# Kernel tuning notes

Measured on AMD Instinct MI355X. Metric: run time of the kernel, lower is better.

Reference implementation:

```python
import jax, jax.numpy as jnp
import numpy as np

N = 50000      # nodes
E = 800000     # edges
IN = 128       # in_channels
H = 128        # hidden_channels
OUT = 500      # out_channels
EPS = 1e-5


def setup_inputs() -> dict:
    key = jax.random.key(0)
    ks = jax.random.split(key, 8)
    def rn(k, shape, scale=0.05):
        return jax.random.normal(k, shape, jnp.float32) * scale
    return {
        "x": jax.random.normal(ks[0], (N, IN), jnp.float32),
        "edge_index": jax.random.randint(ks[1], (2, E), 0, N, dtype=jnp.int32),
        "W1": rn(ks[2], (IN, H)), "b1": jnp.zeros((H,), jnp.float32),
        "g1": jnp.ones((H,), jnp.float32), "be1": jnp.zeros((H,), jnp.float32),
        "W2": rn(ks[3], (H, 2 * H)), "b2": jnp.zeros((2 * H,), jnp.float32),
        "g2": jnp.ones((2 * H,), jnp.float32), "be2": jnp.zeros((2 * H,), jnp.float32),
        "W3": rn(ks[4], (2 * H, H)), "b3": jnp.zeros((H,), jnp.float32),
        "g3": jnp.ones((H,), jnp.float32), "be3": jnp.zeros((H,), jnp.float32),
        "Wl1": rn(ks[5], (H, H // 2)), "bl1": jnp.zeros((H // 2,), jnp.float32),
        "g4": jnp.ones((H // 2,), jnp.float32), "be4": jnp.zeros((H // 2,), jnp.float32),
        "Wl2": rn(ks[6], (H // 2, OUT)), "bl2": jnp.zeros((OUT,), jnp.float32),
    }


def layer_norm(x, g, b):
    mu = jnp.mean(x, axis=-1, keepdims=True)
    var = jnp.mean(jnp.square(x - mu), axis=-1, keepdims=True)
    return (x - mu) * jax.lax.rsqrt(var + EPS) * g + b


def gcn_conv(x, W, b, src, dst, n):
    # PyG GCNConv: x' = D^{-1/2} (A + I) D^{-1/2} (x W) + b, with self-loops.
    h = x @ W                                   # [N, F]
    ones = jnp.ones(src.shape[0], h.dtype)
    deg = jax.ops.segment_sum(ones, dst, num_segments=n) + 1.0  # +1 self-loop
    dinv = jnp.where(deg > 0, jax.lax.rsqrt(deg), 0.0)          # [N]
    coef = dinv[src] * dinv[dst]                # [E]
    agg = jax.ops.segment_sum(h[src] * coef[:, None], dst, num_segments=n)
    agg = agg + h * jnp.square(dinv)[:, None]   # self-loop messages
    return agg + b


def reference(x, edge_index, W1, b1, g1, be1, W2, b2, g2, be2,
              W3, b3, g3, be3, Wl1, bl1, g4, be4, Wl2, bl2):
    # eval mode: dropout is identity
    src, dst = edge_index[0], edge_index[1]
    n = x.shape[0]
    h = jax.nn.elu(layer_norm(gcn_conv(x, W1, b1, src, dst, n), g1, be1))
    h = jax.nn.elu(layer_norm(gcn_conv(h, W2, b2, src, dst, n), g2, be2))
    h = jax.nn.elu(layer_norm(gcn_conv(h, W3, b3, src, dst, n), g3, be3))
    h = jax.nn.elu(layer_norm(h @ Wl1 + bl1, g4, be4))
    return h @ Wl2 + bl2
```

## Files before the change

kernel.cpp:

```cpp
#include <hip/hip_runtime.h>
#include <cstdint>


#define LN_EPS 1e-5f

typedef __attribute__((ext_vector_type(8))) short bf16x8;
typedef __attribute__((ext_vector_type(4))) float f32x4;

static __device__ __forceinline__ ushort f2bf(float f) {
  union { float f; uint u; } c; c.f = f;
  uint u = c.u;
  return (ushort)((u + 0x7fffu + ((u >> 16) & 1u)) >> 16);
}
static __device__ __forceinline__ float bf2f(ushort h) {
  union { uint u; float f; } c; c.u = (uint)h << 16;
  return c.f;
}


__global__ void zero1_kernel(int* __restrict__ a, int n) {
  int i = blockIdx.x * blockDim.x + threadIdx.x;
  if (i < n) a[i] = 0;
}

__global__ void deg_kernel(const int* __restrict__ dst, int* __restrict__ deg, int E) {
  int e = blockIdx.x * blockDim.x + threadIdx.x;
  if (e < E) atomicAdd(&deg[dst[e]], 1);
}

__global__ void scan1_kernel(const int* __restrict__ deg, int* __restrict__ excl,
                             int* __restrict__ bsums, float* __restrict__ dinv, int N) {
  __shared__ int s[256];
  int tid = threadIdx.x;
  int i = blockIdx.x * 256 + tid;
  int v = (i < N) ? deg[i] : 0;
  s[tid] = v;
  __syncthreads();
  for (int o = 1; o < 256; o <<= 1) {
    int t = (tid >= o) ? s[tid - o] : 0;
    __syncthreads();
    if (tid >= o) s[tid] += t;
    __syncthreads();
  }
  if (i < N) {
    excl[i] = s[tid] - v;
    dinv[i] = rsqrtf((float)v + 1.0f);
  }
  if (tid == 255) bsums[blockIdx.x] = s[tid];
}

__global__ void scan2_kernel(int* __restrict__ bsums, int nb) {
  __shared__ int s[256];
  int tid = threadIdx.x;
  int v = (tid < nb) ? bsums[tid] : 0;
  s[tid] = v;
  __syncthreads();
  for (int o = 1; o < 256; o <<= 1) {
    int t = (tid >= o) ? s[tid - o] : 0;
    __syncthreads();
    if (tid >= o) s[tid] += t;
    __syncthreads();
  }
  if (tid < nb) bsums[tid] = s[tid] - v;
}

__global__ void scan3_kernel(int* __restrict__ rowptr, int* __restrict__ fill,
                             const int* __restrict__ bsums, int N, int Etotal) {
  int i = blockIdx.x * blockDim.x + threadIdx.x;
  if (i < N) {
    int v = rowptr[i] + bsums[i >> 8];
    rowptr[i] = v;
    fill[i] = v;
  } else if (i == N) {
    rowptr[N] = Etotal;
  }
}

__global__ void fill_kernel(const int* __restrict__ src, const int* __restrict__ dst,
                            int* __restrict__ fill, int* __restrict__ srcs, int E) {
  int e = blockIdx.x * blockDim.x + threadIdx.x;
  if (e >= E) return;
  int idx = atomicAdd(&fill[dst[e]], 1);
  srcs[idx] = src[e];
}


__global__ void f2bf_vec_kernel(const float* __restrict__ in, ushort* __restrict__ out, int n4) {
  int i = blockIdx.x * blockDim.x + threadIdx.x;
  if (i >= n4) return;
  float4 v = ((const float4*)in)[i];
  ushort4 o;
  o.x = f2bf(v.x); o.y = f2bf(v.y); o.z = f2bf(v.z); o.w = f2bf(v.w);
  ((ushort4*)out)[i] = o;
}

struct WConvArgs {
  const float* w[5];
  ushort* wt[5];
  int K[5], N[5];
  int off[6];
};

__global__ void wconv_kernel(WConvArgs a, int total) {
  int i = blockIdx.x * blockDim.x + threadIdx.x;
  if (i >= total) return;
  int m = 0;
  while (i >= a.off[m + 1]) m++;
  int j = i - a.off[m];
  int k = j / a.N[m], n = j - k * a.N[m];
  a.wt[m][(size_t)n * a.K[m] + k] = f2bf(a.w[m][j]);
}

#define TBM 128
#define TBN 128
#define TBK 32
#define LDK 40

template <bool OUT_BF16>
__global__ __launch_bounds__(256, 2) void mfma_gemm_kernel(
    const ushort* __restrict__ A, const ushort* __restrict__ Bt,
    const float* __restrict__ bias, void* __restrict__ Cout,
    int M, int N, int K) {
  __shared__ ushort As[TBM][LDK];
  __shared__ ushort Bs[TBN][LDK];
  const int tid = threadIdx.x;
  const int lane = tid & 63;
  const int w = tid >> 6;
  const int wm = w & 1, wn = w >> 1;
  const int quad = lane >> 4, l16 = lane & 15;
  const int rowBase = blockIdx.y * TBM;
  const int colBase = blockIdx.x * TBN;

  f32x4 acc[4][4] = {};
  const int lr = tid >> 2;
  const int lk = (tid & 3) * 8;

  for (int k0 = 0; k0 < K; k0 += TBK) {
#pragma unroll
    for (int h = 0; h < 2; h++) {
      int r = lr + h * 64;
      int grow = rowBase + r;
      uint4 va = make_uint4(0, 0, 0, 0);
      if (grow < M) va = *(const uint4*)(A + (size_t)grow * K + k0 + lk);
      *(uint4*)&As[r][lk] = va;
      int gcol = colBase + r;
      uint4 vb = make_uint4(0, 0, 0, 0);
      if (gcol < N) vb = *(const uint4*)(Bt + (size_t)gcol * K + k0 + lk);
      *(uint4*)&Bs[r][lk] = vb;
    }
    __syncthreads();
    bf16x8 af[4], bfr[4];
#pragma unroll
    for (int i = 0; i < 4; i++) {
      af[i]  = *(const bf16x8*)&As[wm * 64 + i * 16 + l16][quad * 8];
      bfr[i] = *(const bf16x8*)&Bs[wn * 64 + i * 16 + l16][quad * 8];
    }
#pragma unroll
    for (int i = 0; i < 4; i++)
#pragma unroll
      for (int j = 0; j < 4; j++)
        acc[i][j] = __builtin_amdgcn_mfma_f32_16x16x32_bf16(af[i], bfr[j], acc[i][j], 0, 0, 0);
    __syncthreads();
  }
#pragma unroll
  for (int i = 0; i < 4; i++) {
    int row0 = rowBase + wm * 64 + i * 16 + quad * 4;
#pragma unroll
    for (int j = 0; j < 4; j++) {
      int col = colBase + wn * 64 + j * 16 + l16;
      if (col >= N) continue;
      float bv = bias ? bias[col] : 0.f;
#pragma unroll
      for (int r = 0; r < 4; r++) {
        int row = row0 + r;
        if (row >= M) continue;
        float v = acc[i][j][r] + bv;
        if (OUT_BF16) ((ushort*)Cout)[(size_t)row * N + col] = f2bf(v);
        else          ((float*)Cout)[(size_t)row * N + col] = v;
      }
    }
  }
}


__global__ __launch_bounds__(256) void agg_kernel(
    const ushort* __restrict__ hb, const int* __restrict__ rowptr,
    const int* __restrict__ srcs, const float* __restrict__ dinv,
    uint* __restrict__ out, int Nn) {
  const int wave = threadIdx.x >> 6;
  const int n = blockIdx.x * 4 + wave;
  if (n >= Nn) return;
  const int f = threadIdx.x & 63;
  const uint* h32 = (const uint*)hb;
  const float di = dinv[n];
  uint self = h32[(size_t)n * 64 + f];
  float a0 = bf2f((ushort)(self & 0xffffu)) * di * di;
  float a1 = bf2f((ushort)(self >> 16)) * di * di;
  int i = rowptr[n];
  const int e = rowptr[n + 1];
  for (; i + 3 < e; i += 4) {
    int s0 = srcs[i], s1 = srcs[i + 1], s2 = srcs[i + 2], s3 = srcs[i + 3];
    float c0 = dinv[s0] * di, c1 = dinv[s1] * di, c2 = dinv[s2] * di, c3 = dinv[s3] * di;
    uint v0 = h32[(size_t)s0 * 64 + f];
    uint v1 = h32[(size_t)s1 * 64 + f];
    uint v2 = h32[(size_t)s2 * 64 + f];
    uint v3 = h32[(size_t)s3 * 64 + f];
    a0 += c0 * bf2f((ushort)(v0 & 0xffffu)) + c1 * bf2f((ushort)(v1 & 0xffffu)) +
          c2 * bf2f((ushort)(v2 & 0xffffu)) + c3 * bf2f((ushort)(v3 & 0xffffu));
    a1 += c0 * bf2f((ushort)(v0 >> 16)) + c1 * bf2f((ushort)(v1 >> 16)) +
          c2 * bf2f((ushort)(v2 >> 16)) + c3 * bf2f((ushort)(v3 >> 16));
  }
  for (; i < e; i++) {
    int s = srcs[i];
    float c = dinv[s] * di;
    uint v = h32[(size_t)s * 64 + f];
    a0 += c * bf2f((ushort)(v & 0xffffu));
    a1 += c * bf2f((ushort)(v >> 16));
  }
  out[(size_t)n * 64 + f] = (uint)f2bf(a0) | ((uint)f2bf(a1) << 16);
}

__global__ __launch_bounds__(256) void agg_ln_kernel(
    const ushort* __restrict__ hb, const int* __restrict__ rowptr,
    const int* __restrict__ srcs, const float* __restrict__ dinv,
    const float* __restrict__ bias, const float* __restrict__ g,
    const float* __restrict__ be, uint* __restrict__ out, int Nn) {
  const int wave = threadIdx.x >> 6;
  const int n = blockIdx.x * 4 + wave;
  if (n >= Nn) return;
  const int f = threadIdx.x & 63;
  const uint* h32 = (const uint*)hb;
  const float di = dinv[n];
  uint self = h32[(size_t)n * 64 + f];
  float2 bv = ((const float2*)bias)[f];
  float a0 = bf2f((ushort)(self & 0xffffu)) * di * di + bv.x;
  float a1 = bf2f((ushort)(self >> 16)) * di * di + bv.y;
  int i = rowptr[n];
  const int e = rowptr[n + 1];
  for (; i + 3 < e; i += 4) {
    int s0 = srcs[i], s1 = srcs[i + 1], s2 = srcs[i + 2], s3 = srcs[i + 3];
    float c0 = dinv[s0] * di, c1 = dinv[s1] * di, c2 = dinv[s2] * di, c3 = dinv[s3] * di;
    uint v0 = h32[(size_t)s0 * 64 + f];
    uint v1 = h32[(size_t)s1 * 64 + f];
    uint v2 = h32[(size_t)s2 * 64 + f];
    uint v3 = h32[(size_t)s3 * 64 + f];
    a0 += c0 * bf2f((ushort)(v0 & 0xffffu)) + c1 * bf2f((ushort)(v1 & 0xffffu)) +
          c2 * bf2f((ushort)(v2 & 0xffffu)) + c3 * bf2f((ushort)(v3 & 0xffffu));
    a1 += c0 * bf2f((ushort)(v0 >> 16)) + c1 * bf2f((ushort)(v1 >> 16)) +
          c2 * bf2f((ushort)(v2 >> 16)) + c3 * bf2f((ushort)(v3 >> 16));
  }
  for (; i < e; i++) {
    int s = srcs[i];
    float c = dinv[s] * di;
    uint v = h32[(size_t)s * 64 + f];
    a0 += c * bf2f((ushort)(v & 0xffffu));
    a1 += c * bf2f((ushort)(v >> 16));
  }
  float s = a0 + a1;
#pragma unroll
  for (int o = 32; o >= 1; o >>= 1) s += __shfl_xor(s, o);
  float mean = s * (1.0f / 128.0f);
  float d0 = a0 - mean, d1 = a1 - mean;
  float q = d0 * d0 + d1 * d1;
#pragma unroll
  for (int o = 32; o >= 1; o >>= 1) q += __shfl_xor(q, o);
  float rstd = rsqrtf(q * (1.0f / 128.0f) + LN_EPS);
  float2 gv = ((const float2*)g)[f];
  float2 bev = ((const float2*)be)[f];
  float y0 = d0 * rstd * gv.x + bev.x;
  float y1 = d1 * rstd * gv.y + bev.y;
  y0 = (y0 > 0.f) ? y0 : expm1f(y0);
  y1 = (y1 > 0.f) ? y1 : expm1f(y1);
  out[(size_t)n * 64 + f] = (uint)f2bf(y0) | ((uint)f2bf(y1) << 16);
}

template <int F, bool IN_BF16>
__global__ __launch_bounds__(F) void ln_elu_kernel(const void* __restrict__ xin,
                                                   const float* __restrict__ g,
                                                   const float* __restrict__ be,
                                                   ushort* __restrict__ out) {
  constexpr int NW = (F + 63) / 64;
  __shared__ float sb[NW];
  const int row = blockIdx.x;
  const int f = threadIdx.x;
  float v;
  if (IN_BF16) v = bf2f(((const ushort*)xin)[(size_t)row * F + f]);
  else         v = ((const float*)xin)[(size_t)row * F + f];
  float s = v;
#pragma unroll
  for (int o = 32; o >= 1; o >>= 1) s += __shfl_xor(s, o);
  float mean;
  if constexpr (NW == 1) {
    mean = s * (1.0f / F);
  } else {
    if ((f & 63) == 0) sb[f >> 6] = s;
    __syncthreads();
    float t = 0.f;
#pragma unroll
    for (int w2 = 0; w2 < NW; w2++) t += sb[w2];
    mean = t * (1.0f / F);
    __syncthreads();
  }
  float d = v - mean;
  float q = d * d;
#pragma unroll
  for (int o = 32; o >= 1; o >>= 1) q += __shfl_xor(q, o);
  float var;
  if constexpr (NW == 1) {
    var = q * (1.0f / F);
  } else {
    if ((f & 63) == 0) sb[f >> 6] = q;
    __syncthreads();
    float t = 0.f;
#pragma unroll
    for (int w2 = 0; w2 < NW; w2++) t += sb[w2];
    var = t * (1.0f / F);
  }
  float y = d * rsqrtf(var + LN_EPS) * g[f] + be[f];
  out[(size_t)row * F + f] = f2bf((y > 0.f) ? y : expm1f(y));
}


extern "C" void kernel_launch(void* const* d_in, const int* in_sizes, int n_in,
                              void* d_out, int out_size, void* d_ws, size_t ws_size,
                              hipStream_t stream) {
  const float* x   = (const float*)d_in[0];
  const int*   ei  = (const int*)d_in[1];
  const float* W1  = (const float*)d_in[2];
  const float* b1  = (const float*)d_in[3];
  const float* g1  = (const float*)d_in[4];
  const float* be1 = (const float*)d_in[5];
  const float* W2  = (const float*)d_in[6];
  const float* b2  = (const float*)d_in[7];
  const float* g2  = (const float*)d_in[8];
  const float* be2 = (const float*)d_in[9];
  const float* W3  = (const float*)d_in[10];
  const float* b3  = (const float*)d_in[11];
  const float* g3  = (const float*)d_in[12];
  const float* be3 = (const float*)d_in[13];
  const float* Wl1 = (const float*)d_in[14];
  const float* bl1 = (const float*)d_in[15];
  const float* g4  = (const float*)d_in[16];
  const float* be4 = (const float*)d_in[17];
  const float* Wl2 = (const float*)d_in[18];
  const float* bl2 = (const float*)d_in[19];

  const int N = in_sizes[0] / 128;
  const int E = in_sizes[1] / 2;
  const int* esrc = ei;
  const int* edst = ei + E;

  char* p = (char*)d_ws;
  float* F1 = (float*)p;              p += (size_t)N * 128 * 4;
  ushort* Pb = (ushort*)p;            p += (size_t)N * 256 * 2;
  ushort* Qb = (ushort*)p;            p += (size_t)N * 256 * 2;
  ushort* W1t = (ushort*)p;           p += 128 * 128 * 2;
  ushort* W2t = (ushort*)p;           p += 128 * 256 * 2;
  ushort* W3t = (ushort*)p;           p += 256 * 128 * 2;
  ushort* Wl1t = (ushort*)p;          p += 128 * 64 * 2;
  ushort* Wl2t = (ushort*)p;          p += 64 * 500 * 2;
  int*   srcs  = (int*)p;             p += (size_t)E * 4;
  int*   deg   = (int*)p;             p += (size_t)N * 4;
  float* dinv  = (float*)p;           p += (size_t)N * 4;
  int*   rowptr= (int*)p;             p += (size_t)(N + 2) * 4;
  int*   fill  = (int*)p;             p += (size_t)N * 4;
  int*   bsums = (int*)p;             p += 256 * 4;
  ushort* xb = (ushort*)F1;

  const int nb = (N + 255) / 256;
  const int eb = (E + 255) / 256;

  zero1_kernel<<<nb, 256, 0, stream>>>(deg, N);
  deg_kernel<<<eb, 256, 0, stream>>>(edst, deg, E);
  scan1_kernel<<<nb, 256, 0, stream>>>(deg, rowptr, bsums, dinv, N);
  scan2_kernel<<<1, 256, 0, stream>>>(bsums, nb);
  scan3_kernel<<<(N + 256) / 256, 256, 0, stream>>>(rowptr, fill, bsums, N, E);
  fill_kernel<<<eb, 256, 0, stream>>>(esrc, edst, fill, srcs, E);

  f2bf_vec_kernel<<<(N * 128 / 4 + 255) / 256, 256, 0, stream>>>(x, xb, N * 128 / 4);
  WConvArgs wa;
  wa.w[0] = W1;  wa.wt[0] = W1t;  wa.K[0] = 128; wa.N[0] = 128;
  wa.w[1] = W2;  wa.wt[1] = W2t;  wa.K[1] = 128; wa.N[1] = 256;
  wa.w[2] = W3;  wa.wt[2] = W3t;  wa.K[2] = 256; wa.N[2] = 128;
  wa.w[3] = Wl1; wa.wt[3] = Wl1t; wa.K[3] = 128; wa.N[3] = 64;
  wa.w[4] = Wl2; wa.wt[4] = Wl2t; wa.K[4] = 64;  wa.N[4] = 500;
  wa.off[0] = 0;
  for (int m = 0; m < 5; m++) wa.off[m + 1] = wa.off[m] + wa.K[m] * wa.N[m];
  int wtotal = wa.off[5];
  wconv_kernel<<<(wtotal + 255) / 256, 256, 0, stream>>>(wa, wtotal);

  auto gemm_bf = [&](const ushort* A, const ushort* Bt, const float* bias, ushort* C,
                     int M, int Nn, int K) {
    dim3 grid((Nn + TBN - 1) / TBN, (M + TBM - 1) / TBM);
    mfma_gemm_kernel<true><<<grid, 256, 0, stream>>>(A, Bt, bias, C, M, Nn, K);
  };
  auto gemm_f32 = [&](const ushort* A, const ushort* Bt, const float* bias, float* C,
                      int M, int Nn, int K) {
    dim3 grid((Nn + TBN - 1) / TBN, (M + TBM - 1) / TBM);
    mfma_gemm_kernel<false><<<grid, 256, 0, stream>>>(A, Bt, bias, C, M, Nn, K);
  };
  const int ab = (N + 3) / 4;

  gemm_bf(xb, W1t, nullptr, Pb, N, 128, 128);
  agg_ln_kernel<<<ab, 256, 0, stream>>>(Pb, rowptr, srcs, dinv, b1, g1, be1, (uint*)Qb, N);

  agg_kernel<<<ab, 256, 0, stream>>>(Qb, rowptr, srcs, dinv, (uint*)Pb, N);
  gemm_bf(Pb, W2t, b2, Qb, N, 256, 128);
  ln_elu_kernel<256, true><<<N, 256, 0, stream>>>(Qb, g2, be2, Pb);

  gemm_bf(Pb, W3t, nullptr, Qb, N, 128, 256);
  agg_ln_kernel<<<ab, 256, 0, stream>>>(Qb, rowptr, srcs, dinv, b3, g3, be3, (uint*)Pb, N);

  gemm_f32(Pb, Wl1t, bl1, F1, N, 64, 128);
  ln_elu_kernel<64, false><<<N, 64, 0, stream>>>(F1, g4, be4, Qb);

  gemm_f32(Qb, Wl2t, bl2, (float*)d_out, N, 500, 64);
}
```

Before: 529.7 us.

## Fuse fp32-to-bf16 input cast into GEMM, vectorize aggregation gathers, repack LN kernels

The first GEMM now reads fp32 x directly and converts to bf16 while staging into shared memory, which removes the separate conversion kernel and its round trip through memory. The aggregation kernels become one template that gives 4 edges per wave, with 16 lanes per edge loading 16-byte uint4 rows, and reduces across lanes with shuffles. This cuts the number of gather instructions but leaves three quarters of the lanes idle at the final store. The 64-wide LayerNorm kernel now packs four rows per block instead of using 64-thread blocks.

```diff
diff --git a/kernel.cpp b/kernel.cpp
--- a/kernel.cpp
+++ b/kernel.cpp
@@ -14,6 +14,14 @@
 }
 static __device__ __forceinline__ float bf2f(ushort h) {
   union { uint u; float f; } c; c.u = (uint)h << 16;
+  return c.f;
+}
+static __device__ __forceinline__ float bflo(uint u) {
+  union { uint u; float f; } c; c.u = u << 16;
+  return c.f;
+}
+static __device__ __forceinline__ float bfhi(uint u) {
+  union { uint u; float f; } c; c.u = u & 0xffff0000u;
   return c.f;
 }
 
@@ -85,15 +93,6 @@
 }
 
 
-__global__ void f2bf_vec_kernel(const float* __restrict__ in, ushort* __restrict__ out, int n4) {
-  int i = blockIdx.x * blockDim.x + threadIdx.x;
-  if (i >= n4) return;
-  float4 v = ((const float4*)in)[i];
-  ushort4 o;
-  o.x = f2bf(v.x); o.y = f2bf(v.y); o.z = f2bf(v.z); o.w = f2bf(v.w);
-  ((ushort4*)out)[i] = o;
-}
-
 struct WConvArgs {
   const float* w[5];
   ushort* wt[5];
@@ -116,9 +115,9 @@
 #define TBK 32
 #define LDK 40
 
-template <bool OUT_BF16>
+template <bool A_FP32, bool OUT_BF16>
 __global__ __launch_bounds__(256, 2) void mfma_gemm_kernel(
-    const ushort* __restrict__ A, const ushort* __restrict__ Bt,
+    const void* __restrict__ Ain, const ushort* __restrict__ Bt,
     const float* __restrict__ bias, void* __restrict__ Cout,
     int M, int N, int K) {
   __shared__ ushort As[TBM][LDK];
@@ -132,21 +131,45 @@
   const int colBase = blockIdx.x * TBN;
 
   f32x4 acc[4][4] = {};
-  const int lr = tid >> 2;
-  const int lk = (tid & 3) * 8;
+  const int sr = tid >> 1;
+  const int sk = (tid & 1) * 16;
 
   for (int k0 = 0; k0 < K; k0 += TBK) {
-#pragma unroll
-    for (int h = 0; h < 2; h++) {
-      int r = lr + h * 64;
-      int grow = rowBase + r;
-      uint4 va = make_uint4(0, 0, 0, 0);
-      if (grow < M) va = *(const uint4*)(A + (size_t)grow * K + k0 + lk);
-      *(uint4*)&As[r][lk] = va;
-      int gcol = colBase + r;
-      uint4 vb = make_uint4(0, 0, 0, 0);
-      if (gcol < N) vb = *(const uint4*)(Bt + (size_t)gcol * K + k0 + lk);
-      *(uint4*)&Bs[r][lk] = vb;
+    {
+      int grow = rowBase + sr;
+      if (A_FP32) {
+        const float* Af = (const float*)Ain;
+        float4 f0 = {}, f1 = {}, f2 = {}, f3 = {};
+        if (grow < M) {
+          const float4* ap = (const float4*)(Af + (size_t)grow * K + k0 + sk);
+          f0 = ap[0]; f1 = ap[1]; f2 = ap[2]; f3 = ap[3];
+        }
+        ushort t[16] = {f2bf(f0.x), f2bf(f0.y), f2bf(f0.z), f2bf(f0.w),
+                        f2bf(f1.x), f2bf(f1.y), f2bf(f1.z), f2bf(f1.w),
+                        f2bf(f2.x), f2bf(f2.y), f2bf(f2.z), f2bf(f2.w),
+                        f2bf(f3.x), f2bf(f3.y), f2bf(f3.z), f2bf(f3.w)};
+        *(uint4*)&As[sr][sk] = *(const uint4*)&t[0];
+        *(uint4*)&As[sr][sk + 8] = *(const uint4*)&t[8];
+      } else {
+        const ushort* Ab = (const ushort*)Ain;
+        uint4 v0 = {}, v1 = {};
+        if (grow < M) {
+          const uint4* ap = (const uint4*)(Ab + (size_t)grow * K + k0 + sk);
+          v0 = ap[0]; v1 = ap[1];
+        }
+        *(uint4*)&As[sr][sk] = v0;
+        *(uint4*)&As[sr][sk + 8] = v1;
+      }
+    }
+    {
+      int gcol = colBase + sr;
+      uint4 v0 = {}, v1 = {};
+      if (gcol < N) {
+        const uint4* bp = (const uint4*)(Bt + (size_t)gcol * K + k0 + sk);
+        v0 = bp[0]; v1 = bp[1];
+      }
+      *(uint4*)&Bs[sr][sk] = v0;
+      *(uint4*)&Bs[sr][sk + 8] = v1;
     }
     __syncthreads();
     bf16x8 af[4], bfr[4];
@@ -182,45 +205,8 @@
   }
 }
 
-
+template <bool DO_LN>
 __global__ __launch_bounds__(256) void agg_kernel(
-    const ushort* __restrict__ hb, const int* __restrict__ rowptr,
-    const int* __restrict__ srcs, const float* __restrict__ dinv,
-    uint* __restrict__ out, int Nn) {
-  const int wave = threadIdx.x >> 6;
-  const int n = blockIdx.x * 4 + wave;
-  if (n >= Nn) return;
-  const int f = threadIdx.x & 63;
-  const uint* h32 = (const uint*)hb;
-  const float di = dinv[n];
-  uint self = h32[(size_t)n * 64 + f];
-  float a0 = bf2f((ushort)(self & 0xffffu)) * di * di;
-  float a1 = bf2f((ushort)(self >> 16)) * di * di;
-  int i = rowptr[n];
-  const int e = rowptr[n + 1];
-  for (; i + 3 < e; i += 4) {
-    int s0 = srcs[i], s1 = srcs[i + 1], s2 = srcs[i + 2], s3 = srcs[i + 3];
-    float c0 = dinv[s0] * di, c1 = dinv[s1] * di, c2 = dinv[s2] * di, c3 = dinv[s3] * di;
-    uint v0 = h32[(size_t)s0 * 64 + f];
-    uint v1 = h32[(size_t)s1 * 64 + f];
-    uint v2 = h32[(size_t)s2 * 64 + f];
-    uint v3 = h32[(size_t)s3 * 64 + f];
-    a0 += c0 * bf2f((ushort)(v0 & 0xffffu)) + c1 * bf2f((ushort)(v1 & 0xffffu)) +
-          c2 * bf2f((ushort)(v2 & 0xffffu)) + c3 * bf2f((ushort)(v3 & 0xffffu));
-    a1 += c0 * bf2f((ushort)(v0 >> 16)) + c1 * bf2f((ushort)(v1 >> 16)) +
-          c2 * bf2f((ushort)(v2 >> 16)) + c3 * bf2f((ushort)(v3 >> 16));
-  }
-  for (; i < e; i++) {
-    int s = srcs[i];
-    float c = dinv[s] * di;
-    uint v = h32[(size_t)s * 64 + f];
-    a0 += c * bf2f((ushort)(v & 0xffffu));
-    a1 += c * bf2f((ushort)(v >> 16));
-  }
-  out[(size_t)n * 64 + f] = (uint)f2bf(a0) | ((uint)f2bf(a1) << 16);
-}
-
-__global__ __launch_bounds__(256) void agg_ln_kernel(
     const ushort* __restrict__ hb, const int* __restrict__ rowptr,
     const int* __restrict__ srcs, const float* __restrict__ dinv,
     const float* __restrict__ bias, const float* __restrict__ g,
@@ -228,96 +214,128 @@
   const int wave = threadIdx.x >> 6;
   const int n = blockIdx.x * 4 + wave;
   if (n >= Nn) return;
-  const int f = threadIdx.x & 63;
-  const uint* h32 = (const uint*)hb;
+  const int lane = threadIdx.x & 63;
+  const int slot = lane >> 4;
+  const int sl = lane & 15;
   const float di = dinv[n];
-  uint self = h32[(size_t)n * 64 + f];
-  float2 bv = ((const float2*)bias)[f];
-  float a0 = bf2f((ushort)(self & 0xffffu)) * di * di + bv.x;
-  float a1 = bf2f((ushort)(self >> 16)) * di * di + bv.y;
-  int i = rowptr[n];
-  const int e = rowptr[n + 1];
-  for (; i + 3 < e; i += 4) {
-    int s0 = srcs[i], s1 = srcs[i + 1], s2 = srcs[i + 2], s3 = srcs[i + 3];
-    float c0 = dinv[s0] * di, c1 = dinv[s1] * di, c2 = dinv[s2] * di, c3 = dinv[s3] * di;
-    uint v0 = h32[(size_t)s0 * 64 + f];
-    uint v1 = h32[(size_t)s1 * 64 + f];
-    uint v2 = h32[(size_t)s2 * 64 + f];
-    uint v3 = h32[(size_t)s3 * 64 + f];
-    a0 += c0 * bf2f((ushort)(v0 & 0xffffu)) + c1 * bf2f((ushort)(v1 & 0xffffu)) +
-          c2 * bf2f((ushort)(v2 & 0xffffu)) + c3 * bf2f((ushort)(v3 & 0xffffu));
-    a1 += c0 * bf2f((ushort)(v0 >> 16)) + c1 * bf2f((ushort)(v1 >> 16)) +
-          c2 * bf2f((ushort)(v2 >> 16)) + c3 * bf2f((ushort)(v3 >> 16));
-  }
-  for (; i < e; i++) {
-    int s = srcs[i];
-    float c = dinv[s] * di;
-    uint v = h32[(size_t)s * 64 + f];
-    a0 += c * bf2f((ushort)(v & 0xffffu));
-    a1 += c * bf2f((ushort)(v >> 16));
-  }
-  float s = a0 + a1;
-#pragma unroll
-  for (int o = 32; o >= 1; o >>= 1) s += __shfl_xor(s, o);
-  float mean = s * (1.0f / 128.0f);
-  float d0 = a0 - mean, d1 = a1 - mean;
-  float q = d0 * d0 + d1 * d1;
-#pragma unroll
-  for (int o = 32; o >= 1; o >>= 1) q += __shfl_xor(q, o);
-  float rstd = rsqrtf(q * (1.0f / 128.0f) + LN_EPS);
-  float2 gv = ((const float2*)g)[f];
-  float2 bev = ((const float2*)be)[f];
-  float y0 = d0 * rstd * gv.x + bev.x;
-  float y1 = d1 * rstd * gv.y + bev.y;
-  y0 = (y0 > 0.f) ? y0 : expm1f(y0);
-  y1 = (y1 > 0.f) ? y1 : expm1f(y1);
-  out[(size_t)n * 64 + f] = (uint)f2bf(y0) | ((uint)f2bf(y1) << 16);
-}
-
-template <int F, bool IN_BF16>
-__global__ __launch_bounds__(F) void ln_elu_kernel(const void* __restrict__ xin,
-                                                   const float* __restrict__ g,
-                                                   const float* __restrict__ be,
-                                                   ushort* __restrict__ out) {
-  constexpr int NW = (F + 63) / 64;
-  __shared__ float sb[NW];
+
+  float acc[8] = {};
+  {
+    uint4 v = ((const uint4*)(hb + (size_t)n * 128))[sl];
+    float c = (slot == 0) ? di * di : 0.f;
+    acc[0] = c * bflo(v.x); acc[1] = c * bfhi(v.x);
+    acc[2] = c * bflo(v.y); acc[3] = c * bfhi(v.y);
+    acc[4] = c * bflo(v.z); acc[5] = c * bfhi(v.z);
+    acc[6] = c * bflo(v.w); acc[7] = c * bfhi(v.w);
+  }
+  const int e0 = rowptr[n], e1 = rowptr[n + 1];
+  for (int i = e0; i < e1; i += 8) {
+    int i0 = i + slot, i1 = i + 4 + slot;
+    int s0 = (i0 < e1) ? srcs[i0] : 0;
+    int s1 = (i1 < e1) ? srcs[i1] : 0;
+    float c0 = (i0 < e1) ? dinv[s0] * di : 0.f;
+    float c1 = (i1 < e1) ? dinv[s1] * di : 0.f;
+    uint4 v0 = ((const uint4*)(hb + (size_t)s0 * 128))[sl];
+    uint4 v1 = ((const uint4*)(hb + (size_t)s1 * 128))[sl];
+    acc[0] += c0 * bflo(v0.x) + c1 * bflo(v1.x);
+    acc[1] += c0 * bfhi(v0.x) + c1 * bfhi(v1.x);
+    acc[2] += c0 * bflo(v0.y) + c1 * bflo(v1.y);
+    acc[3] += c0 * bfhi(v0.y) + c1 * bfhi(v1.y);
+    acc[4] += c0 * bflo(v0.z) + c1 * bflo(v1.z);
+    acc[5] += c0 * bfhi(v0.z) + c1 * bfhi(v1.z);
+    acc[6] += c0 * bflo(v0.w) + c1 * bflo(v1.w);
+    acc[7] += c0 * bfhi(v0.w) + c1 * bfhi(v1.w);
+  }
+#pragma unroll
+  for (int j = 0; j < 8; j++) {
+    acc[j] += __shfl_xor(acc[j], 16);
+    acc[j] += __shfl_xor(acc[j], 32);
+  }
+  if (DO_LN) {
+    float4 bv0 = ((const float4*)bias)[2 * sl];
+    float4 bv1 = ((const float4*)bias)[2 * sl + 1];
+    acc[0] += bv0.x; acc[1] += bv0.y; acc[2] += bv0.z; acc[3] += bv0.w;
+    acc[4] += bv1.x; acc[5] += bv1.y; acc[6] += bv1.z; acc[7] += bv1.w;
+    float s = acc[0] + acc[1] + acc[2] + acc[3] + acc[4] + acc[5] + acc[6] + acc[7];
+#pragma unroll
+    for (int o = 1; o <= 8; o <<= 1) s += __shfl_xor(s, o);
+    float mean = s * (1.0f / 128.0f);
+    float q = 0.f;
+#pragma unroll
+    for (int j = 0; j < 8; j++) {
+      acc[j] -= mean;
+      q += acc[j] * acc[j];
+    }
+#pragma unroll
+    for (int o = 1; o <= 8; o <<= 1) q += __shfl_xor(q, o);
+    float rstd = rsqrtf(q * (1.0f / 128.0f) + LN_EPS);
+    float4 gv0 = ((const float4*)g)[2 * sl];
+    float4 gv1 = ((const float4*)g)[2 * sl + 1];
+    float4 ev0 = ((const float4*)be)[2 * sl];
+    float4 ev1 = ((const float4*)be)[2 * sl + 1];
+    float gg[8] = {gv0.x, gv0.y, gv0.z, gv0.w, gv1.x, gv1.y, gv1.z, gv1.w};
+    float ee[8] = {ev0.x, ev0.y, ev0.z, ev0.w, ev1.x, ev1.y, ev1.z, ev1.w};
+#pragma unroll
+    for (int j = 0; j < 8; j++) {
+      float y = acc[j] * rstd * gg[j] + ee[j];
+      acc[j] = (y > 0.f) ? y : expm1f(y);
+    }
+  }
+  if (slot == 0) {
+    uint4 o;
+    o.x = (uint)f2bf(acc[0]) | ((uint)f2bf(acc[1]) << 16);
+    o.y = (uint)f2bf(acc[2]) | ((uint)f2bf(acc[3]) << 16);
+    o.z = (uint)f2bf(acc[4]) | ((uint)f2bf(acc[5]) << 16);
+    o.w = (uint)f2bf(acc[6]) | ((uint)f2bf(acc[7]) << 16);
+    ((uint4*)(out + (size_t)n * 64))[sl] = o;
+  }
+}
+
+
+__global__ __launch_bounds__(256) void ln_elu256_kernel(const ushort* __restrict__ xin,
+                                                        const float* __restrict__ g,
+                                                        const float* __restrict__ be,
+                                                        ushort* __restrict__ out) {
+  __shared__ float sb[4];
   const int row = blockIdx.x;
   const int f = threadIdx.x;
-  float v;
-  if (IN_BF16) v = bf2f(((const ushort*)xin)[(size_t)row * F + f]);
-  else         v = ((const float*)xin)[(size_t)row * F + f];
+  float v = bf2f(xin[(size_t)row * 256 + f]);
   float s = v;
 #pragma unroll
   for (int o = 32; o >= 1; o >>= 1) s += __shfl_xor(s, o);
-  float mean;
-  if constexpr (NW == 1) {
-    mean = s * (1.0f / F);
-  } else {
-    if ((f & 63) == 0) sb[f >> 6] = s;
-    __syncthreads();
-    float t = 0.f;
-#pragma unroll
-    for (int w2 = 0; w2 < NW; w2++) t += sb[w2];
-    mean = t * (1.0f / F);
-    __syncthreads();
-  }
+  if ((f & 63) == 0) sb[f >> 6] = s;
+  __syncthreads();
+  float mean = (sb[0] + sb[1] + sb[2] + sb[3]) * (1.0f / 256.0f);
+  __syncthreads();
   float d = v - mean;
   float q = d * d;
 #pragma unroll
   for (int o = 32; o >= 1; o >>= 1) q += __shfl_xor(q, o);
-  float var;
-  if constexpr (NW == 1) {
-    var = q * (1.0f / F);
-  } else {
-    if ((f & 63) == 0) sb[f >> 6] = q;
-    __syncthreads();
-    float t = 0.f;
-#pragma unroll
-    for (int w2 = 0; w2 < NW; w2++) t += sb[w2];
-    var = t * (1.0f / F);
-  }
+  if ((f & 63) == 0) sb[f >> 6] = q;
+  __syncthreads();
+  float var = (sb[0] + sb[1] + sb[2] + sb[3]) * (1.0f / 256.0f);
   float y = d * rsqrtf(var + LN_EPS) * g[f] + be[f];
-  out[(size_t)row * F + f] = f2bf((y > 0.f) ? y : expm1f(y));
+  out[(size_t)row * 256 + f] = f2bf((y > 0.f) ? y : expm1f(y));
+}
+
+__global__ __launch_bounds__(256) void ln_elu64_kernel(const float* __restrict__ xin,
+                                                       const float* __restrict__ g,
+                                                       const float* __restrict__ be,
+                                                       ushort* __restrict__ out, int Nn) {
+  const int n = blockIdx.x * 4 + (threadIdx.x >> 6);
+  if (n >= Nn) return;
+  const int f = threadIdx.x & 63;
+  float v = xin[(size_t)n * 64 + f];
+  float s = v;
+#pragma unroll
+  for (int o = 32; o >= 1; o >>= 1) s += __shfl_xor(s, o);
+  float mean = s * (1.0f / 64.0f);
+  float d = v - mean;
+  float q = d * d;
+#pragma unroll
+  for (int o = 32; o >= 1; o >>= 1) q += __shfl_xor(q, o);
+  float y = d * rsqrtf(q * (1.0f / 64.0f) + LN_EPS) * g[f] + be[f];
+  out[(size_t)n * 64 + f] = f2bf((y > 0.f) ? y : expm1f(y));
 }
 
 
@@ -365,7 +383,6 @@
   int*   rowptr= (int*)p;             p += (size_t)(N + 2) * 4;
   int*   fill  = (int*)p;             p += (size_t)N * 4;
   int*   bsums = (int*)p;             p += 256 * 4;
-  ushort* xb = (ushort*)F1;
 
   const int nb = (N + 255) / 256;
   const int eb = (E + 255) / 256;
@@ -377,7 +394,6 @@
   scan3_kernel<<<(N + 256) / 256, 256, 0, stream>>>(rowptr, fill, bsums, N, E);
   fill_kernel<<<eb, 256, 0, stream>>>(esrc, edst, fill, srcs, E);
 
-  f2bf_vec_kernel<<<(N * 128 / 4 + 255) / 256, 256, 0, stream>>>(x, xb, N * 128 / 4);
   WConvArgs wa;
   wa.w[0] = W1;  wa.wt[0] = W1t;  wa.K[0] = 128; wa.N[0] = 128;
   wa.w[1] = W2;  wa.wt[1] = W2t;  wa.K[1] = 128; wa.N[1] = 256;
@@ -389,30 +405,35 @@
   int wtotal = wa.off[5];
   wconv_kernel<<<(wtotal + 255) / 256, 256, 0, stream>>>(wa, wtotal);
 
-  auto gemm_bf = [&](const ushort* A, const ushort* Bt, const float* bias, ushort* C,
-                     int M, int Nn, int K) {
-    dim3 grid((Nn + TBN - 1) / TBN, (M + TBM - 1) / TBM);
-    mfma_gemm_kernel<true><<<grid, 256, 0, stream>>>(A, Bt, bias, C, M, Nn, K);
-  };
-  auto gemm_f32 = [&](const ushort* A, const ushort* Bt, const float* bias, float* C,
-                      int M, int Nn, int K) {
-    dim3 grid((Nn + TBN - 1) / TBN, (M + TBM - 1) / TBM);
-    mfma_gemm_kernel<false><<<grid, 256, 0, stream>>>(A, Bt, bias, C, M, Nn, K);
-  };
   const int ab = (N + 3) / 4;
 
-  gemm_bf(xb, W1t, nullptr, Pb, N, 128, 128);
-  agg_ln_kernel<<<ab, 256, 0, stream>>>(Pb, rowptr, srcs, dinv, b1, g1, be1, (uint*)Qb, N);
-
-  agg_kernel<<<ab, 256, 0, stream>>>(Qb, rowptr, srcs, dinv, (uint*)Pb, N);
-  gemm_bf(Pb, W2t, b2, Qb, N, 256, 128);
-  ln_elu_kernel<256, true><<<N, 256, 0, stream>>>(Qb, g2, be2, Pb);
-
-  gemm_bf(Pb, W3t, nullptr, Qb, N, 128, 256);
-  agg_ln_kernel<<<ab, 256, 0, stream>>>(Qb, rowptr, srcs, dinv, b3, g3, be3, (uint*)Pb, N);
-
-  gemm_f32(Pb, Wl1t, bl1, F1, N, 64, 128);
-  ln_elu_kernel<64, false><<<N, 64, 0, stream>>>(F1, g4, be4, Qb);
-
-  gemm_f32(Qb, Wl2t, bl2, (float*)d_out, N, 500, 64);
-}
+  {
+    dim3 grid((128 + TBN - 1) / TBN, (N + TBM - 1) / TBM);
+    mfma_gemm_kernel<true, true><<<grid, 256, 0, stream>>>(x, W1t, nullptr, Pb, N, 128, 128);
+  }
+  agg_kernel<true><<<ab, 256, 0, stream>>>(Pb, rowptr, srcs, dinv, b1, g1, be1, (uint*)Qb, N);
+
+  agg_kernel<false><<<ab, 256, 0, stream>>>(Qb, rowptr, srcs, dinv, nullptr, nullptr, nullptr, (uint*)Pb, N);
+  {
+    dim3 grid((256 + TBN - 1) / TBN, (N + TBM - 1) / TBM);
+    mfma_gemm_kernel<false, true><<<grid, 256, 0, stream>>>(Pb, W2t, b2, Qb, N, 256, 128);
+  }
+  ln_elu256_kernel<<<N, 256, 0, stream>>>(Qb, g2, be2, Pb);
+
+  {
+    dim3 grid((128 + TBN - 1) / TBN, (N + TBM - 1) / TBM);
+    mfma_gemm_kernel<false, true><<<grid, 256, 0, stream>>>(Pb, W3t, nullptr, Qb, N, 128, 256);
+  }
+  agg_kernel<true><<<ab, 256, 0, stream>>>(Qb, rowptr, srcs, dinv, b3, g3, be3, (uint*)Pb, N);
+
+  {
+    dim3 grid((64 + TBN - 1) / TBN, (N + TBM - 1) / TBM);
+    mfma_gemm_kernel<false, false><<<grid, 256, 0, stream>>>(Pb, Wl1t, bl1, F1, N, 64, 128);
+  }
+  ln_elu64_kernel<<<ab, 256, 0, stream>>>(F1, g4, be4, Qb, N);
+
+  {
+    dim3 grid((500 + TBN - 1) / TBN, (N + TBM - 1) / TBM);
+    mfma_gemm_kernel<false, false><<<grid, 256, 0, stream>>>(Qb, Wl2t, bl2, d_out, N, 500, 64);
+  }
+}
```

Result: no change. 534.1 us (+0.8%).
